# Performance work log

Measured on AMD Instinct MI355X. Metric: run time of the kernel, lower is better.

Reference implementation:

```python
import jax, jax.numpy as jnp
import numpy as np

DIM = 2048
N_HEADS = 16
HEAD_DIM = DIM // N_HEADS
GROUP_SIZE = 128
THRESHOLD = 0.5
EPS = 1e-8
B, T = 2, 2048


def _ternary_dequant(w):
    # groupwise absmean ternary quantize + dequant; DIM % GROUP_SIZE == 0 so no pad
    O, I = w.shape
    g = I // GROUP_SIZE
    wg = w.reshape(O, g, GROUP_SIZE)
    scale = jnp.clip(jnp.mean(jnp.abs(wg), axis=-1, keepdims=True), EPS)
    wn = wg / scale
    q = jnp.where(wn > THRESHOLD, 1.0, jnp.where(wn < -THRESHOLD, -1.0, 0.0))
    return (q * scale).reshape(O, I)


def _bitlinear(x, w):
    # STE: forward uses quantized weight
    w_ste = w + jax.lax.stop_gradient(_ternary_dequant(w) - w)
    return x @ w_ste.T


def _rope_tables(t, head_dim, base=10000.0):
    half = head_dim // 2
    inv_freq = 1.0 / (base ** (jnp.arange(half, dtype=jnp.float32) / half))
    freqs = jnp.outer(jnp.arange(t, dtype=jnp.float32), inv_freq)  # [T, half]
    return jnp.cos(freqs), jnp.sin(freqs)


def _apply_rope(x, cos, sin):
    # x: [B, H, T, D]
    d = x.shape[-1]
    x1, x2 = x[..., : d // 2], x[..., d // 2 :]
    cos = cos[None, None, :, :]
    sin = sin[None, None, :, :]
    return jnp.concatenate([x1 * cos - x2 * sin, x1 * sin + x2 * cos], axis=-1)


def setup_inputs() -> dict:
    key = jax.random.key(0)
    ks = jax.random.split(key, 5)
    std = 1.0 / np.sqrt(DIM)
    return {
        "x": jax.random.normal(ks[0], (B, T, DIM), dtype=jnp.float32),
        "w_q": jax.random.normal(ks[1], (DIM, DIM), dtype=jnp.float32) * std,
        "w_k": jax.random.normal(ks[2], (DIM, DIM), dtype=jnp.float32) * std,
        "w_v": jax.random.normal(ks[3], (DIM, DIM), dtype=jnp.float32) * std,
        "w_o": jax.random.normal(ks[4], (DIM, DIM), dtype=jnp.float32) * std,
    }


def reference(x, w_q, w_k, w_v, w_o):
    b, t, c = x.shape
    scale = HEAD_DIM ** -0.5

    def split_heads(y):
        return y.reshape(b, t, N_HEADS, HEAD_DIM).transpose(0, 2, 1, 3)  # [B,H,T,D]

    q = split_heads(_bitlinear(x, w_q))
    k = split_heads(_bitlinear(x, w_k))
    v = split_heads(_bitlinear(x, w_v))

    cos, sin = _rope_tables(t, HEAD_DIM)
    q = _apply_rope(q, cos, sin)
    k = _apply_rope(k, cos, sin)

    scores = jnp.einsum("bhqd,bhkd->bhqk", q, k) * scale
    causal = jnp.triu(jnp.ones((t, t), dtype=bool), k=1)
    scores = jnp.where(causal[None, None], -jnp.inf, scores)
    probs = jax.nn.softmax(scores, axis=-1)
    y = jnp.einsum("bhqk,bhkd->bhqd", probs, v)
    y = y.transpose(0, 2, 1, 3).reshape(b, t, c)
    return _bitlinear(y, w_o)
```

## Files before the change

kernel.cpp:

```cpp
#include <hip/hip_runtime.h>
#include <stdint.h>
#include <math.h>

#define DIMC 2048
#define NHEADS 16
#define HDIM 128
#define TSEQ 2048
#define NTOK 4096

using bf16x8 = __attribute__((ext_vector_type(8))) short;
using f32x4  = __attribute__((ext_vector_type(4))) float;

typedef __attribute__((address_space(1))) const void gas_void;
typedef __attribute__((address_space(3))) void las_void;

static __device__ __forceinline__ unsigned short f2b(float f) {
  union { float f; unsigned int u; } a; a.f = f;
  unsigned int u = a.u;
  u = (u + 0x7fffu + ((u >> 16) & 1u)) >> 16;
  return (unsigned short)u;
}
static __device__ __forceinline__ float b2f(unsigned short s) {
  union { unsigned int u; float f; } a; a.u = ((unsigned int)s) << 16;
  return a.f;
}

__global__ void detect_dtype(const unsigned short* __restrict__ xs,
                             int* __restrict__ flag)
{
  const int lane = threadIdx.x;
  const unsigned short u = xs[2 * lane];
  const int e = (u >> 7) & 0xFF;
  const bool plausible = (e >= 112) && (e <= 135);
  const unsigned long long m = __ballot(plausible);
  if (lane == 0) *flag = (__popcll(m) >= 32) ? 1 : 0;
}

static __device__ __forceinline__ void dequant_one(
    const void* __restrict__ w, unsigned short* __restrict__ o,
    int grp, int lane, int isbf16)
{
  float a, bq;
  if (isbf16) {
    const unsigned int pk =
        ((const unsigned int*)((const unsigned short*)w + (long)grp * 128))[lane];
    a  = b2f((unsigned short)(pk & 0xffffu));
    bq = b2f((unsigned short)(pk >> 16));
  } else {
    const float2 v = ((const float2*)((const float*)w + (long)grp * 128))[lane];
    a = v.x; bq = v.y;
  }
  double s = fabs((double)a) + fabs((double)bq);
  #pragma unroll
  for (int off = 1; off < 64; off <<= 1) s += __shfl_xor(s, off);
  double scale = s * (1.0 / 128.0);
  if (scale < 1e-8) scale = 1e-8;
  const float fs = (float)scale;
  const double wn0 = (double)a / scale;
  const double wn1 = (double)bq / scale;
  const float q0 = (wn0 > 0.5) ? fs : ((wn0 < -0.5) ? -fs : 0.0f);
  const float q1 = (wn1 > 0.5) ? fs : ((wn1 < -0.5) ? -fs : 0.0f);
  const unsigned int opk = (unsigned int)f2b(q0) | ((unsigned int)f2b(q1) << 16);
  ((unsigned int*)o)[(long)grp * 64 + lane] = opk;
}

__global__ void __launch_bounds__(256) dequant_auto(
    const void* __restrict__ w, unsigned short* __restrict__ o,
    const int* __restrict__ flag)
{
  const int wave = threadIdx.x >> 6, lane = threadIdx.x & 63;
  dequant_one(w, o, blockIdx.x * 4 + wave, lane, *flag);
}

__global__ void __launch_bounds__(256) dequant3(
    const void* __restrict__ w0, const void* __restrict__ w1,
    const void* __restrict__ w2, unsigned short* __restrict__ o,
    const int* __restrict__ flag)
{
  const int wave = threadIdx.x >> 6, lane = threadIdx.x & 63;
  const void* w = (blockIdx.y == 0) ? w0 : (blockIdx.y == 1) ? w1 : w2;
  unsigned short* oo = o + (long)blockIdx.y * DIMC * DIMC;
  dequant_one(w, oo, blockIdx.x * 4 + wave, lane, *flag);
}

__global__ void __launch_bounds__(256) cast_auto(
    const void* __restrict__ x, unsigned short* __restrict__ o,
    const int* __restrict__ flag)
{
  const int i = (blockIdx.x * 256 + threadIdx.x) * 4;
  if (*flag) {
    *(ushort4*)(o + i) = *(const ushort4*)((const unsigned short*)x + i);
  } else {
    const float4 v = *(const float4*)((const float*)x + i);
    ushort4 u;
    u.x = f2b(v.x); u.y = f2b(v.y); u.z = f2b(v.z); u.w = f2b(v.w);
    *(ushort4*)(o + i) = u;
  }
}

__device__ __forceinline__ void storeOne(float* C, long i, float v) { C[i] = v; }
__device__ __forceinline__ void storeOne(unsigned short* C, long i, float v) { C[i] = f2b(v); }

template <typename OUTT>
static __device__ __forceinline__ void gemm_tile(
    const unsigned short* __restrict__ A, const unsigned short* __restrict__ B,
    OUTT* __restrict__ C, int m0, int n0, int Nc, int K,
    unsigned short* As, unsigned short* Bs)
{
  const int tid = threadIdx.x;
  const int wave = tid >> 6;
  const int lane = tid & 63;
  const int wr = (wave >> 1) * 64, wc = (wave & 1) * 64;
  const int c16 = lane & 15, q4 = lane >> 4;

  f32x4 acc[4][4];
  #pragma unroll
  for (int i = 0; i < 4; i++)
    #pragma unroll
    for (int j = 0; j < 4; j++)
      acc[i][j] = (f32x4){0.f, 0.f, 0.f, 0.f};

  const int srow = tid >> 2;
  const int scol = (tid & 3) * 8;
  const unsigned short* ga = A + (long)(m0 + srow) * K + scol;
  const unsigned short* gb = B + (long)(n0 + srow) * K + scol;

  for (int k0 = 0; k0 < K; k0 += 32) {
    #pragma unroll
    for (int i = 0; i < 2; i++) {
      __builtin_amdgcn_global_load_lds(
          (gas_void*)(ga + (long)i * 64 * K + k0),
          (las_void*)(As + i * 2048 + wave * 512), 16, 0, 0);
      __builtin_amdgcn_global_load_lds(
          (gas_void*)(gb + (long)i * 64 * K + k0),
          (las_void*)(Bs + i * 2048 + wave * 512), 16, 0, 0);
    }
    __syncthreads();
    bf16x8 af[4], bfr[4];
    #pragma unroll
    for (int t = 0; t < 4; t++) {
      af[t]  = *(const bf16x8*)(As + (wr + t * 16 + c16) * 32 + q4 * 8);
      bfr[t] = *(const bf16x8*)(Bs + (wc + t * 16 + c16) * 32 + q4 * 8);
    }
    #pragma unroll
    for (int mt = 0; mt < 4; mt++)
      #pragma unroll
      for (int nt = 0; nt < 4; nt++)
        acc[mt][nt] = __builtin_amdgcn_mfma_f32_16x16x32_bf16(af[mt], bfr[nt], acc[mt][nt], 0, 0, 0);
    __syncthreads();
  }

  #pragma unroll
  for (int mt = 0; mt < 4; mt++) {
    const int m = m0 + wr + mt * 16 + q4 * 4;
    #pragma unroll
    for (int nt = 0; nt < 4; nt++) {
      const int n = wc + nt * 16 + c16;
      #pragma unroll
      for (int r = 0; r < 4; r++)
        storeOne(C, (long)(m + r) * Nc + n, acc[mt][nt][r]);
    }
  }
}

template <typename OUTT>
__global__ void __launch_bounds__(256) gemm_bt(
    const unsigned short* __restrict__ A, const unsigned short* __restrict__ B,
    OUTT* __restrict__ C, int M, int N, int K)
{
  __shared__ unsigned short As[128 * 32];
  __shared__ unsigned short Bs[128 * 32];
  gemm_tile<OUTT>(A, B, C + blockIdx.x * 128, blockIdx.y * 128, blockIdx.x * 128,
                  N, K, As, Bs);
}

__global__ void __launch_bounds__(256) gemm_qkv(
    const unsigned short* __restrict__ A, const unsigned short* __restrict__ B,
    unsigned short* __restrict__ C0, unsigned short* __restrict__ C1,
    unsigned short* __restrict__ C2, int K)
{
  __shared__ unsigned short As[128 * 32];
  __shared__ unsigned short Bs[128 * 32];
  const int n0 = blockIdx.x * 128;
  unsigned short* Cb = (n0 < 2048) ? C0 : (n0 < 4096) ? C1 : C2;
  gemm_tile<unsigned short>(A, B, Cb + (n0 & 2047), blockIdx.y * 128, n0,
                            DIMC, K, As, Bs);
}

__global__ void __launch_bounds__(256) rope_kernel(
    unsigned short* __restrict__ Q, unsigned short* __restrict__ Kb)
{
  const int idx = blockIdx.x * 256 + threadIdx.x;
  const int d = idx & 63;
  const int h = (idx >> 6) & (NHEADS - 1);
  const int row = idx >> 10;
  const int t = row & (TSEQ - 1);
  const float inv_freq = expf(-9.210340371976184f * (float)d * (1.0f / 64.0f));
  float sn, cs;
  sincosf((float)t * inv_freq, &sn, &cs);
  const long base = (long)row * DIMC + h * HDIM + d;
  float x1 = b2f(Q[base]), x2 = b2f(Q[base + 64]);
  Q[base]      = f2b(x1 * cs - x2 * sn);
  Q[base + 64] = f2b(x1 * sn + x2 * cs);
  x1 = b2f(Kb[base]); x2 = b2f(Kb[base + 64]);
  Kb[base]      = f2b(x1 * cs - x2 * sn);
  Kb[base + 64] = f2b(x1 * sn + x2 * cs);
}

#define FA_M 16.0f
__global__ void __launch_bounds__(256) fattn(
    const unsigned short* __restrict__ Q,
    const unsigned short* __restrict__ K,
    const unsigned short* __restrict__ V,
    unsigned short* __restrict__ Y)
{
  __shared__ unsigned short SU[9216];
  __shared__ unsigned short VT[128 * 72];
  __shared__ float red[4][32];

  const int tid = threadIdx.x, wave = tid >> 6, lane = tid & 63;
  const int idx = blockIdx.x;
  const int qt = 15 - (idx >> 5);
  const int bh = idx & 31;
  const int b = bh >> 4, h = bh & 15;
  const int qbase = qt * 128;
  const int qw = wave * 32;
  const int c = lane & 15, g = lane >> 4;
  const long tokbase = (long)b * TSEQ;
  const int col0 = h * HDIM;

  bf16x8 qf[2][4];
  #pragma unroll
  for (int qq = 0; qq < 2; qq++) {
    const unsigned short* qp =
        Q + (tokbase + qbase + qw + qq * 16 + c) * DIMC + col0 + g * 8;
    #pragma unroll
    for (int kc = 0; kc < 4; kc++) qf[qq][kc] = *(const bf16x8*)(qp + kc * 32);
  }

  f32x4 od[8][2];
  #pragma unroll
  for (int dt = 0; dt < 8; dt++)
    #pragma unroll
    for (int qq = 0; qq < 2; qq++)
      od[dt][qq] = (f32x4){0.f, 0.f, 0.f, 0.f};
  float lpart[2][4];
  #pragma unroll
  for (int qq = 0; qq < 2; qq++)
    #pragma unroll
    for (int r = 0; r < 4; r++) lpart[qq][r] = 0.0f;

  const int ksr = tid >> 2, ksc = (tid & 3) * 32;
  const int vk0 = (tid & 31) * 2, vd0 = (tid >> 5) * 16;

  const float SC = 0.088388347648318447f;
  const int nkt = 2 * qt + 2;
  for (int kt = 0; kt < nkt; kt++) {
    const int kb = kt * 64;
    __syncthreads();
    {
      const unsigned short* src = K + (tokbase + kb + ksr) * DIMC + col0 + ksc;
      float4* dst = (float4*)&SU[ksr * 136 + ksc];
      dst[0] = ((const float4*)src)[0];
      dst[1] = ((const float4*)src)[1];
      dst[2] = ((const float4*)src)[2];
      dst[3] = ((const float4*)src)[3];
    }
    {
      const unsigned short* s0 = V + (tokbase + kb + vk0) * DIMC + col0 + vd0;
      const unsigned short* s1 = s0 + DIMC;
      bf16x8 a0 = *(const bf16x8*)(s0);
      bf16x8 a1 = *(const bf16x8*)(s0 + 8);
      bf16x8 b0 = *(const bf16x8*)(s1);
      bf16x8 b1 = *(const bf16x8*)(s1 + 8);
      #pragma unroll
      for (int dd = 0; dd < 8; dd++) {
        const unsigned int p0 =
            (unsigned int)(unsigned short)a0[dd] |
            ((unsigned int)(unsigned short)b0[dd] << 16);
        *(unsigned int*)&VT[(vd0 + dd) * 72 + vk0] = p0;
      }
      #pragma unroll
      for (int dd = 0; dd < 8; dd++) {
        const unsigned int p1 =
            (unsigned int)(unsigned short)a1[dd] |
            ((unsigned int)(unsigned short)b1[dd] << 16);
        *(unsigned int*)&VT[(vd0 + 8 + dd) * 72 + vk0] = p1;
      }
    }
    __syncthreads();

    f32x4 sacc[2][4];
    #pragma unroll
    for (int qq = 0; qq < 2; qq++)
      #pragma unroll
      for (int nt = 0; nt < 4; nt++) sacc[qq][nt] = (f32x4){0.f, 0.f, 0.f, 0.f};
    #pragma unroll
    for (int kc = 0; kc < 4; kc++) {
      bf16x8 bk[4];
      #pragma unroll
      for (int nt = 0; nt < 4; nt++)
        bk[nt] = *(const bf16x8*)&SU[(nt * 16 + c) * 136 + kc * 32 + g * 8];
      #pragma unroll
      for (int qq = 0; qq < 2; qq++)
        #pragma unroll
        for (int nt = 0; nt < 4; nt++)
          sacc[qq][nt] = __builtin_amdgcn_mfma_f32_16x16x32_bf16(
              qf[qq][kc], bk[nt], sacc[qq][nt], 0, 0, 0);
    }
    __syncthreads();

    #pragma unroll
    for (int qq = 0; qq < 2; qq++)
      #pragma unroll
      for (int r = 0; r < 4; r++) {
        const int qg = qbase + qw + qq * 16 + g * 4 + r;
        #pragma unroll
        for (int nt = 0; nt < 4; nt++) {
          const int kg = kb + nt * 16 + c;
          const float sv = sacc[qq][nt][r] * SC - FA_M;
          const float p = (kg > qg) ? 0.0f : __expf(sv);
          lpart[qq][r] += p;
          SU[(wave * 32 + qq * 16 + g * 4 + r) * 72 + nt * 16 + c] = f2b(p);
        }
      }

    #pragma unroll
    for (int kc = 0; kc < 2; kc++) {
      bf16x8 pb[2];
      #pragma unroll
      for (int qq = 0; qq < 2; qq++)
        pb[qq] = *(const bf16x8*)&SU[(wave * 32 + qq * 16 + c) * 72 + kc * 32 + g * 8];
      #pragma unroll
      for (int dt = 0; dt < 8; dt++) {
        bf16x8 va = *(const bf16x8*)&VT[(dt * 16 + c) * 72 + kc * 32 + g * 8];
        #pragma unroll
        for (int qq = 0; qq < 2; qq++)
          od[dt][qq] = __builtin_amdgcn_mfma_f32_16x16x32_bf16(
              va, pb[qq], od[dt][qq], 0, 0, 0);
      }
    }
  }

  #pragma unroll
  for (int qq = 0; qq < 2; qq++)
    #pragma unroll
    for (int r = 0; r < 4; r++) {
      float l = lpart[qq][r];
      #pragma unroll
      for (int off = 1; off < 16; off <<= 1) l += __shfl_xor(l, off);
      lpart[qq][r] = l;
    }
  __syncthreads();
  if (c == 0) {
    #pragma unroll
    for (int qq = 0; qq < 2; qq++)
      #pragma unroll
      for (int r = 0; r < 4; r++)
        red[wave][qq * 16 + g * 4 + r] = 1.0f / lpart[qq][r];
  }
  __syncthreads();
  #pragma unroll
  for (int qq = 0; qq < 2; qq++) {
    const float linv = red[wave][qq * 16 + c];
    unsigned short* yp =
        Y + (tokbase + qbase + qw + qq * 16 + c) * DIMC + col0;
    #pragma unroll
    for (int dt = 0; dt < 8; dt++)
      #pragma unroll
      for (int r = 0; r < 4; r++)
        yp[dt * 16 + g * 4 + r] = f2b(od[dt][qq][r] * linv);
  }
}

extern "C" void kernel_launch(void* const* d_in, const int* in_sizes, int n_in,
                              void* d_out, int out_size, void* d_ws, size_t ws_size,
                              hipStream_t stream)
{
  const void* x  = d_in[0];
  const void* wq = d_in[1];
  const void* wk = d_in[2];
  const void* wv = d_in[3];
  const void* wo = d_in[4];
  float* out = (float*)d_out;

  char* ws = (char*)d_ws;
  const size_t MB = 1024 * 1024;
  unsigned short* wbuf = (unsigned short*)(ws + 0 * MB);
  unsigned short* xb   = (unsigned short*)(ws + 24 * MB);
  unsigned short* Qb   = (unsigned short*)(ws + 40 * MB);
  unsigned short* Kb   = (unsigned short*)(ws + 56 * MB);
  unsigned short* Vb   = (unsigned short*)(ws + 72 * MB);
  int* flag            = (int*)(ws + 88 * MB);
  unsigned short* Yb   = xb;

  detect_dtype<<<dim3(1), 64, 0, stream>>>((const unsigned short*)x, flag);
  cast_auto<<<dim3(8192), 256, 0, stream>>>(x, xb, flag);
  dequant3<<<dim3(8192, 3), 256, 0, stream>>>(wq, wk, wv, wbuf, flag);
  gemm_qkv<<<dim3(48, 32), 256, 0, stream>>>(xb, wbuf, Qb, Kb, Vb, DIMC);
  rope_kernel<<<dim3(16384), 256, 0, stream>>>(Qb, Kb);
  fattn<<<dim3(512), 256, 0, stream>>>(Qb, Kb, Vb, Yb);
  dequant_auto<<<dim3(8192), 256, 0, stream>>>(wo, wbuf, flag);
  gemm_bt<float><<<dim3(16, 32), 256, 0, stream>>>(Yb, wbuf, out, NTOK, DIMC, DIMC);
}
```

Baseline: 458.5 us.

## Double K-depth of GEMM tiles and register-prefetch next K/V tile in attention

The GEMM main loop now loads a 64-wide K slab (two 32-wide halves) per barrier pair instead of 32, which halves the number of __syncthreads and doubles LDS per block. The attention kernel prefetches the next K and V tile into registers right after the LDS stores, so global loads overlap with the current tile's MFMA work. The cost is more LDS in the GEMM and more registers in attention, which may lower occupancy.

```diff
diff --git a/kernel.cpp b/kernel.cpp
--- a/kernel.cpp
+++ b/kernel.cpp
@@ -125,28 +125,33 @@
   const unsigned short* ga = A + (long)(m0 + srow) * K + scol;
   const unsigned short* gb = B + (long)(n0 + srow) * K + scol;
 
-  for (int k0 = 0; k0 < K; k0 += 32) {
-    #pragma unroll
-    for (int i = 0; i < 2; i++) {
-      __builtin_amdgcn_global_load_lds(
-          (gas_void*)(ga + (long)i * 64 * K + k0),
-          (las_void*)(As + i * 2048 + wave * 512), 16, 0, 0);
-      __builtin_amdgcn_global_load_lds(
-          (gas_void*)(gb + (long)i * 64 * K + k0),
-          (las_void*)(Bs + i * 2048 + wave * 512), 16, 0, 0);
-    }
+  for (int k0 = 0; k0 < K; k0 += 64) {
+    #pragma unroll
+    for (int h = 0; h < 2; h++)
+      #pragma unroll
+      for (int i = 0; i < 2; i++) {
+        __builtin_amdgcn_global_load_lds(
+            (gas_void*)(ga + (long)i * 64 * K + k0 + h * 32),
+            (las_void*)(As + h * 4096 + i * 2048 + wave * 512), 16, 0, 0);
+        __builtin_amdgcn_global_load_lds(
+            (gas_void*)(gb + (long)i * 64 * K + k0 + h * 32),
+            (las_void*)(Bs + h * 4096 + i * 2048 + wave * 512), 16, 0, 0);
+      }
     __syncthreads();
-    bf16x8 af[4], bfr[4];
-    #pragma unroll
-    for (int t = 0; t < 4; t++) {
-      af[t]  = *(const bf16x8*)(As + (wr + t * 16 + c16) * 32 + q4 * 8);
-      bfr[t] = *(const bf16x8*)(Bs + (wc + t * 16 + c16) * 32 + q4 * 8);
-    }
-    #pragma unroll
-    for (int mt = 0; mt < 4; mt++)
-      #pragma unroll
-      for (int nt = 0; nt < 4; nt++)
-        acc[mt][nt] = __builtin_amdgcn_mfma_f32_16x16x32_bf16(af[mt], bfr[nt], acc[mt][nt], 0, 0, 0);
+    #pragma unroll
+    for (int kc = 0; kc < 2; kc++) {
+      bf16x8 af[4], bfr[4];
+      #pragma unroll
+      for (int t = 0; t < 4; t++) {
+        af[t]  = *(const bf16x8*)(As + kc * 4096 + (wr + t * 16 + c16) * 32 + q4 * 8);
+        bfr[t] = *(const bf16x8*)(Bs + kc * 4096 + (wc + t * 16 + c16) * 32 + q4 * 8);
+      }
+      #pragma unroll
+      for (int mt = 0; mt < 4; mt++)
+        #pragma unroll
+        for (int nt = 0; nt < 4; nt++)
+          acc[mt][nt] = __builtin_amdgcn_mfma_f32_16x16x32_bf16(af[mt], bfr[nt], acc[mt][nt], 0, 0, 0);
+    }
     __syncthreads();
   }
 
@@ -168,8 +173,8 @@
     const unsigned short* __restrict__ A, const unsigned short* __restrict__ B,
     OUTT* __restrict__ C, int M, int N, int K)
 {
-  __shared__ unsigned short As[128 * 32];
-  __shared__ unsigned short Bs[128 * 32];
+  __shared__ unsigned short As[128 * 64];
+  __shared__ unsigned short Bs[128 * 64];
   gemm_tile<OUTT>(A, B, C + blockIdx.x * 128, blockIdx.y * 128, blockIdx.x * 128,
                   N, K, As, Bs);
 }
@@ -179,8 +184,8 @@
     unsigned short* __restrict__ C0, unsigned short* __restrict__ C1,
     unsigned short* __restrict__ C2, int K)
 {
-  __shared__ unsigned short As[128 * 32];
-  __shared__ unsigned short Bs[128 * 32];
+  __shared__ unsigned short As[128 * 64];
+  __shared__ unsigned short Bs[128 * 64];
   const int n0 = blockIdx.x * 128;
   unsigned short* Cb = (n0 < 2048) ? C0 : (n0 < 4096) ? C1 : C2;
   gemm_tile<unsigned short>(A, B, Cb + (n0 & 2047), blockIdx.y * 128, n0,
@@ -255,40 +260,54 @@
 
   const float SC = 0.088388347648318447f;
   const int nkt = 2 * qt + 2;
+
+  float4 kr0, kr1, kr2, kr3;
+  bf16x8 va0, va1, vb0, vb1;
+  {
+    const unsigned short* src = K + (tokbase + ksr) * DIMC + col0 + ksc;
+    kr0 = ((const float4*)src)[0]; kr1 = ((const float4*)src)[1];
+    kr2 = ((const float4*)src)[2]; kr3 = ((const float4*)src)[3];
+    const unsigned short* s0 = V + (tokbase + vk0) * DIMC + col0 + vd0;
+    const unsigned short* s1 = s0 + DIMC;
+    va0 = *(const bf16x8*)(s0); va1 = *(const bf16x8*)(s0 + 8);
+    vb0 = *(const bf16x8*)(s1); vb1 = *(const bf16x8*)(s1 + 8);
+  }
+
   for (int kt = 0; kt < nkt; kt++) {
     const int kb = kt * 64;
     __syncthreads();
     {
-      const unsigned short* src = K + (tokbase + kb + ksr) * DIMC + col0 + ksc;
       float4* dst = (float4*)&SU[ksr * 136 + ksc];
-      dst[0] = ((const float4*)src)[0];
-      dst[1] = ((const float4*)src)[1];
-      dst[2] = ((const float4*)src)[2];
-      dst[3] = ((const float4*)src)[3];
+      dst[0] = kr0; dst[1] = kr1; dst[2] = kr2; dst[3] = kr3;
     }
     {
-      const unsigned short* s0 = V + (tokbase + kb + vk0) * DIMC + col0 + vd0;
-      const unsigned short* s1 = s0 + DIMC;
-      bf16x8 a0 = *(const bf16x8*)(s0);
-      bf16x8 a1 = *(const bf16x8*)(s0 + 8);
-      bf16x8 b0 = *(const bf16x8*)(s1);
-      bf16x8 b1 = *(const bf16x8*)(s1 + 8);
       #pragma unroll
       for (int dd = 0; dd < 8; dd++) {
         const unsigned int p0 =
-            (unsigned int)(unsigned short)a0[dd] |
-            ((unsigned int)(unsigned short)b0[dd] << 16);
+            (unsigned int)(unsigned short)va0[dd] |
+            ((unsigned int)(unsigned short)vb0[dd] << 16);
         *(unsigned int*)&VT[(vd0 + dd) * 72 + vk0] = p0;
       }
       #pragma unroll
       for (int dd = 0; dd < 8; dd++) {
         const unsigned int p1 =
-            (unsigned int)(unsigned short)a1[dd] |
-            ((unsigned int)(unsigned short)b1[dd] << 16);
+            (unsigned int)(unsigned short)va1[dd] |
+            ((unsigned int)(unsigned short)vb1[dd] << 16);
         *(unsigned int*)&VT[(vd0 + 8 + dd) * 72 + vk0] = p1;
       }
     }
     __syncthreads();
+
+    if (kt + 1 < nkt) {
+      const int kb2 = kb + 64;
+      const unsigned short* src = K + (tokbase + kb2 + ksr) * DIMC + col0 + ksc;
+      kr0 = ((const float4*)src)[0]; kr1 = ((const float4*)src)[1];
+      kr2 = ((const float4*)src)[2]; kr3 = ((const float4*)src)[3];
+      const unsigned short* s0 = V + (tokbase + kb2 + vk0) * DIMC + col0 + vd0;
+      const unsigned short* s1 = s0 + DIMC;
+      va0 = *(const bf16x8*)(s0); va1 = *(const bf16x8*)(s0 + 8);
+      vb0 = *(const bf16x8*)(s1); vb1 = *(const bf16x8*)(s1 + 8);
+    }
 
     f32x4 sacc[2][4];
     #pragma unroll
```

Measured after the change: 408.2 us. -11.0%, faster.
